# Performance work log

Hardware: AMD Instinct MI355X
Metric: run time of the kernel (lower is better)

## Reference

```python
import jax, jax.numpy as jnp
import numpy as np

B, T, E, A = 4, 4096, 512, 64

def setup_inputs() -> dict:
    key = jax.random.key(0)
    k1, k2, k3, k4 = jax.random.split(key, 4)
    embedded = jax.random.normal(k1, (B, T, E), dtype=jnp.float32)
    # torch Linear(E, A, bias=False): weight [A, E], y = x @ W.T. Store as [E, A].
    s = 1.0 / np.sqrt(E)
    Wq = jax.random.uniform(k2, (E, A), dtype=jnp.float32, minval=-s, maxval=s)
    Wk = jax.random.uniform(k3, (E, A), dtype=jnp.float32, minval=-s, maxval=s)
    Wv = jax.random.uniform(k4, (E, A), dtype=jnp.float32, minval=-s, maxval=s)
    return {"embedded": embedded, "Wq": Wq, "Wk": Wk, "Wv": Wv}

def reference(embedded, Wq, Wk, Wv):
    Q = embedded @ Wq  # [B, T, A]
    K = embedded @ Wk
    V = embedded @ Wv
    A_dim = V.shape[-1]
    scores = jnp.einsum('btd,bsd->bts', Q, K) / jnp.sqrt(jnp.float32(A_dim))  # [B, T, T]
    Tlen = scores.shape[-1]
    causal = jnp.tril(jnp.ones((Tlen, Tlen), dtype=bool))
    scores = jnp.where(causal, scores, -jnp.inf)
    attn = jax.nn.softmax(scores, axis=-1)
    out = jnp.einsum('bts,bsd->btd', attn, V)  # [B, T, A]
    return jnp.round(out, 4)
```

## Files before the change

kernel.cpp:

```cpp
#include <hip/hip_runtime.h>

#define B_ 4
#define T_ 4096
#define E_ 512
#define A_ 64
#define SQSCALE 0.1803368801111204f

typedef __attribute__((ext_vector_type(8)))  short bf16x8;
typedef __attribute__((ext_vector_type(8)))  unsigned short ushort8;
typedef __attribute__((ext_vector_type(4)))  unsigned int   u32x4;
typedef __attribute__((ext_vector_type(4)))  float f32x4;
typedef __attribute__((ext_vector_type(16))) float f32x16;

__device__ __forceinline__ unsigned short f2bf(float x) {
    union { float f; unsigned int u; } v; v.f = x;
    unsigned int r = v.u + 0x7fffu + ((v.u >> 16) & 1u);
    return (unsigned short)(r >> 16);
}
__device__ __forceinline__ unsigned cvtpk(float a, float b) {
    unsigned r;
    asm("v_cvt_pk_bf16_f32 %0, %1, %2" : "=v"(r) : "v"(a), "v"(b));
    return r;
}
__device__ __forceinline__ void pls(unsigned &a, unsigned &b) {
    asm("v_permlane32_swap_b32 %0, %1" : "+v"(a), "+v"(b));
}

__global__ __launch_bounds__(256) void prep_w(
    const float* __restrict__ Wq, const float* __restrict__ Wk,
    const float* __restrict__ Wv, unsigned short* __restrict__ Wp)
{
    const int e = blockIdx.x * 256 + threadIdx.x;
    const int nt = e >> 10;
    const int ks = (e >> 6) & 15;
    const int l  = e & 63;
    const int col = nt * 16 + (l & 15);
    const int kb  = ks * 32 + (l >> 4) * 8;
    const float* W = (col < 64) ? Wq : ((col < 128) ? Wk : Wv);
    const int cc = col & 63;
    const float sc = (col < 64) ? SQSCALE : 1.f;
    union { unsigned short s[8]; ushort8 v; } u;
    #pragma unroll
    for (int j = 0; j < 8; ++j) u.s[j] = f2bf(W[(kb + j) * 64 + cc] * sc);
    *(ushort8*)&Wp[(size_t)e * 8] = u.v;
}

__global__ __launch_bounds__(512, 4) void qkv_proj_kernel(
    const float* __restrict__ emb, const unsigned short* __restrict__ Wp,
    unsigned short* __restrict__ Qp, unsigned short* __restrict__ Kp,
    unsigned short* __restrict__ Vp)
{
    __shared__ unsigned short at[32][536];
    __shared__ unsigned short qt[32][72];
    __shared__ unsigned short kt[32][72];
    __shared__ unsigned short vt[64][40];
    const int tid = threadIdx.x;
    const long row0 = (long)blockIdx.x * 32;

    {
        const int r = tid >> 4, c16 = tid & 15;
        const float* __restrict__ src = emb + (row0 + r) * 512;
        #pragma unroll
        for (int j = 0; j < 4; ++j) {
            const int col = j * 128 + c16 * 8;
            const float4 x0 = *(const float4*)(src + col);
            const float4 x1 = *(const float4*)(src + col + 4);
            u32x4 p;
            p[0] = cvtpk(x0.x, x0.y); p[1] = cvtpk(x0.z, x0.w);
            p[2] = cvtpk(x1.x, x1.y); p[3] = cvtpk(x1.z, x1.w);
            *(u32x4*)&at[r][col] = p;
        }
    }
    __syncthreads();

    const int w = tid >> 6, lane = tid & 63;
    const int c = lane & 15, hi = lane >> 4;
    const int rg = w & 1, ng = w >> 1;

    f32x4 acc[3];
    #pragma unroll
    for (int j = 0; j < 3; ++j) acc[j] = (f32x4){0.f, 0.f, 0.f, 0.f};

    #pragma unroll
    for (int ks = 0; ks < 16; ++ks) {
        const bf16x8 af = *(const bf16x8*)&at[rg * 16 + c][ks * 32 + hi * 8];
        #pragma unroll
        for (int j = 0; j < 3; ++j) {
            const int nt = ng * 3 + j;
            const bf16x8 bf_ = *(const bf16x8*)&Wp[((size_t)(nt * 16 + ks) * 64 + lane) * 8];
            acc[j] = __builtin_amdgcn_mfma_f32_16x16x32_bf16(af, bf_, acc[j], 0, 0, 0);
        }
    }

    #pragma unroll
    for (int j = 0; j < 3; ++j) {
        const int nt = ng * 3 + j;
        #pragma unroll
        for (int r4 = 0; r4 < 4; ++r4) {
            const int rloc = rg * 16 + hi * 4 + r4;
            const unsigned short v = f2bf(acc[j][r4]);
            if (nt < 4)       qt[rloc][nt * 16 + c] = v;
            else if (nt < 8)  kt[rloc][(nt - 4) * 16 + c] = v;
            else              vt[(nt - 8) * 16 + c][rloc] = v;
        }
    }
    __syncthreads();

    const int tloc = (int)(row0 & 4095);
    const long bb = row0 >> 12;
    const int ci  = tloc >> 6;
    const int f_  = (tloc >> 5) & 1;
    const int ks0 = (tloc >> 4) & 3;
    const int tt  = tloc >> 5;
    if (tid < 256) {
        const int kk = tid >> 6, l = tid & 63;
        const ushort8 kval = *(const ushort8*)&kt[l & 31][kk * 16 + (l >> 5) * 8];
        *(ushort8*)&Kp[((((bb * 64 + ci) * 2 + f_) * 4 + kk) * 64 + l) * 8] = kval;
        const ushort8 qval = *(const ushort8*)&qt[l & 31][kk * 16 + (l >> 5) * 8];
        *(ushort8*)&Qp[(((bb * 128 + tt) * 4 + kk) * 64 + l) * 8] = qval;
    } else {
        const int e = tid - 256;
        const int ksl = e >> 7, ct = (e >> 6) & 1, l = e & 63;
        const ushort8 val = *(const ushort8*)&vt[ct * 32 + (l & 31)][ksl * 16 + (l >> 5) * 8];
        *(ushort8*)&Vp[((((bb * 64 + ci) * 4 + ks0 + ksl) * 2 + ct) * 64 + l) * 8] = val;
    }
}

__global__ __launch_bounds__(512, 2) void attn_kernel(
    const unsigned short* __restrict__ Qp, const unsigned short* __restrict__ Kp,
    const unsigned short* __restrict__ Vp, float* __restrict__ out)
{
    __shared__ float accbuf[8][32][68];
    __shared__ float mbuf[8][32], lbuf[8][32];

    const int tid = threadIdx.x, w = tid >> 6, lane = tid & 63;
    const int c = lane & 31, h = lane >> 5;
    const int b = (blockIdx.x & 7) >> 1;
    const int u = ((blockIdx.x >> 3) << 1) | (blockIdx.x & 1);
    const int t = (u < 64) ? (127 - u) : (u - 64);
    const int qb = t << 5;

    const unsigned short* __restrict__ Qpb = Qp + (size_t)b * 128 * 4 * 512;
    const unsigned short* __restrict__ Kpb = Kp + (size_t)b * 64 * 8 * 512;
    const unsigned short* __restrict__ Vpb = Vp + (size_t)b * 64 * 8 * 512;

    bf16x8 qf[4];
    #pragma unroll
    for (int kk = 0; kk < 4; ++kk)
        qf[kk] = *(const bf16x8*)&Qpb[(((size_t)t * 4 + kk) * 64 + lane) * 8];

    f32x16 acc[2];
    #pragma unroll
    for (int ct = 0; ct < 2; ++ct)
        #pragma unroll
        for (int j = 0; j < 16; ++j) acc[ct][j] = 0.f;
    float m = -1e30f, l = 0.f;

    const int nc = ((qb + 31) >> 6) + 1;

    bf16x8 kf[2][4];
    {
        const size_t cp = (w < nc) ? w : (nc - 1);
        #pragma unroll
        for (int f = 0; f < 2; ++f)
            #pragma unroll
            for (int kk = 0; kk < 4; ++kk)
                kf[f][kk] = *(const bf16x8*)&Kpb[(((cp * 2 + f) * 4 + kk) * 64 + lane) * 8];
    }

    for (int ci = w; ci < nc; ci += 8) {
        const long s0 = (long)ci << 6;

        bf16x8 vf[4][2];
        #pragma unroll
        for (int ks = 0; ks < 4; ++ks)
            #pragma unroll
            for (int ct = 0; ct < 2; ++ct)
                vf[ks][ct] = *(const bf16x8*)&Vpb[((((size_t)ci * 4 + ks) * 2 + ct) * 64 + lane) * 8];

        f32x16 sf[2];
        #pragma unroll
        for (int f = 0; f < 2; ++f)
            #pragma unroll
            for (int j = 0; j < 16; ++j) sf[f][j] = 0.f;
        __builtin_amdgcn_s_setprio(1);
        #pragma unroll
        for (int f = 0; f < 2; ++f)
            #pragma unroll
            for (int kk = 0; kk < 4; ++kk)
                sf[f] = __builtin_amdgcn_mfma_f32_32x32x16_bf16(kf[f][kk], qf[kk], sf[f], 0, 0, 0);
        __builtin_amdgcn_s_setprio(0);

        bf16x8 kn[2][4];
        {
            const int cin = ci + 8;
            const size_t cp = (cin < nc) ? cin : (nc - 1);
            #pragma unroll
            for (int f = 0; f < 2; ++f)
                #pragma unroll
                for (int kk = 0; kk < 4; ++kk)
                    kn[f][kk] = *(const bf16x8*)&Kpb[(((cp * 2 + f) * 4 + kk) * 64 + lane) * 8];
        }

        if ((int)s0 + 63 > qb) {
            #pragma unroll
            for (int f = 0; f < 2; ++f)
                #pragma unroll
                for (int r = 0; r < 16; ++r) {
                    const int key = (int)s0 + f * 32 + ((r & 3) + 8 * (r >> 2)) + 4 * h;
                    if (key > qb + c) sf[f][r] = -1e30f;
                }
        }

        float t0 = fmaxf(sf[0][0], sf[1][0]);
        float t1 = fmaxf(sf[0][1], sf[1][1]);
        float t2 = fmaxf(sf[0][2], sf[1][2]);
        float t3 = fmaxf(sf[0][3], sf[1][3]);
        #pragma unroll
        for (int r = 4; r < 16; r += 4) {
            t0 = fmaxf(t0, fmaxf(sf[0][r],     sf[1][r]));
            t1 = fmaxf(t1, fmaxf(sf[0][r + 1], sf[1][r + 1]));
            t2 = fmaxf(t2, fmaxf(sf[0][r + 2], sf[1][r + 2]));
            t3 = fmaxf(t3, fmaxf(sf[0][r + 3], sf[1][r + 3]));
        }
        float pm = fmaxf(fmaxf(t0, t1), fmaxf(t2, t3));
        pm = fmaxf(pm, __shfl_xor(pm, 32));

        float mn = m;
        if (__any(pm > m)) {
            mn = fmaxf(m, pm);
            const float sc = exp2f(m - mn);
            m = mn;
            l *= sc;
            #pragma unroll
            for (int ct = 0; ct < 2; ++ct)
                #pragma unroll
                for (int r = 0; r < 16; ++r) acc[ct][r] *= sc;
        }

        float s0a = 0.f, s1a = 0.f, s2a = 0.f, s3a = 0.f;
        #pragma unroll
        for (int f = 0; f < 2; ++f)
            #pragma unroll
            for (int r = 0; r < 16; r += 4) {
                float p0 = exp2f(sf[f][r] - mn);
                float p1 = exp2f(sf[f][r + 1] - mn);
                float p2 = exp2f(sf[f][r + 2] - mn);
                float p3 = exp2f(sf[f][r + 3] - mn);
                sf[f][r] = p0; sf[f][r + 1] = p1; sf[f][r + 2] = p2; sf[f][r + 3] = p3;
                s0a += p0; s1a += p1; s2a += p2; s3a += p3;
            }
        float rs = (s0a + s1a) + (s2a + s3a);
        rs += __shfl_xor(rs, 32);
        l += rs;

        #pragma unroll
        for (int f = 0; f < 2; ++f) {
            unsigned w01 = cvtpk(sf[f][0], sf[f][1]);
            unsigned w23 = cvtpk(sf[f][2], sf[f][3]);
            unsigned w45 = cvtpk(sf[f][4], sf[f][5]);
            unsigned w67 = cvtpk(sf[f][6], sf[f][7]);
            pls(w01, w45); pls(w23, w67);
            union { unsigned uu[4]; bf16x8 v; } pa0, pa1;
            pa0.uu[0] = w01; pa0.uu[1] = w23; pa0.uu[2] = w45; pa0.uu[3] = w67;
            unsigned x01 = cvtpk(sf[f][8],  sf[f][9]);
            unsigned x23 = cvtpk(sf[f][10], sf[f][11]);
            unsigned x45 = cvtpk(sf[f][12], sf[f][13]);
            unsigned x67 = cvtpk(sf[f][14], sf[f][15]);
            pls(x01, x45); pls(x23, x67);
            pa1.uu[0] = x01; pa1.uu[1] = x23; pa1.uu[2] = x45; pa1.uu[3] = x67;
            __builtin_amdgcn_s_setprio(1);
            #pragma unroll
            for (int ct = 0; ct < 2; ++ct) {
                acc[ct] = __builtin_amdgcn_mfma_f32_32x32x16_bf16(vf[2 * f][ct],     pa0.v, acc[ct], 0, 0, 0);
                acc[ct] = __builtin_amdgcn_mfma_f32_32x32x16_bf16(vf[2 * f + 1][ct], pa1.v, acc[ct], 0, 0, 0);
            }
            __builtin_amdgcn_s_setprio(0);
        }

        #pragma unroll
        for (int f = 0; f < 2; ++f)
            #pragma unroll
            for (int kk = 0; kk < 4; ++kk) kf[f][kk] = kn[f][kk];
    }

    if (h == 0) { mbuf[w][c] = m; lbuf[w][c] = l; }
    #pragma unroll
    for (int ct = 0; ct < 2; ++ct)
        #pragma unroll
        for (int g = 0; g < 4; ++g)
            *(float4*)&accbuf[w][c][ct * 32 + g * 8 + 4 * h] =
                make_float4(acc[ct][4 * g], acc[ct][4 * g + 1],
                            acc[ct][4 * g + 2], acc[ct][4 * g + 3]);
    __syncthreads();
    #pragma unroll
    for (int i = 0; i < 4; ++i) {
        const int e = tid + i * 512;
        const int q = e >> 6, d = e & 63;
        float ms = mbuf[0][q];
        #pragma unroll
        for (int wv = 1; wv < 8; ++wv) ms = fmaxf(ms, mbuf[wv][q]);
        float ls = 0.f, os = 0.f;
        #pragma unroll
        for (int wv = 0; wv < 8; ++wv) {
            const float e_ = exp2f(mbuf[wv][q] - ms);
            ls += lbuf[wv][q] * e_;
            os += accbuf[wv][q][d] * e_;
        }
        out[((long)b * T_ + qb + q) * 64 + d] = os / ls;
    }
}

extern "C" void kernel_launch(void* const* d_in, const int* in_sizes, int n_in,
                              void* d_out, int out_size, void* d_ws, size_t ws_size,
                              hipStream_t stream)
{
    const float* emb = (const float*)d_in[0];
    const float* Wq  = (const float*)d_in[1];
    const float* Wk  = (const float*)d_in[2];
    const float* Wv  = (const float*)d_in[3];
    float* out = (float*)d_out;

    unsigned short* Qp = (unsigned short*)d_ws;
    unsigned short* Kp = Qp + (size_t)B_ * T_ * A_;
    unsigned short* Vp = Kp + (size_t)B_ * T_ * A_;
    unsigned short* Wp = Vp + (size_t)B_ * T_ * A_;

    prep_w<<<dim3(48), dim3(256), 0, stream>>>(Wq, Wk, Wv, Wp);
    qkv_proj_kernel<<<dim3(512), dim3(512), 0, stream>>>(emb, Wp, Qp, Kp, Vp);
    attn_kernel<<<dim3(512), dim3(512), 0, stream>>>(Qp, Kp, Vp, out);
}
```

Measured before the change: 52.02 us.

## Split attention KV range across two blocks and merge partials in a separate kernel

Splits the attention kernel into a flash-decoding style split-K: 1024 blocks each cover alternating groups of 8 key chunks (stride 16), write unnormalized partial accumulators plus max and sum to workspace, and a new merge kernel combines the two halves. This is meant to improve load balance and occupancy over the causal triangle, where long query tiles dominated a 512-block grid. It drops the heavy-first tile ordering and adds an extra launch plus global round-trip of partials. Blocks for short query tiles in the second half may do no work yet still write partials with m=-1e30, l=0.

```diff
diff --git a/kernel.cpp b/kernel.cpp
--- a/kernel.cpp
+++ b/kernel.cpp
@@ -126,18 +126,20 @@
     }
 }
 
-__global__ __launch_bounds__(512, 2) void attn_kernel(
+__global__ __launch_bounds__(512, 2) void attn_part(
     const unsigned short* __restrict__ Qp, const unsigned short* __restrict__ Kp,
-    const unsigned short* __restrict__ Vp, float* __restrict__ out)
+    const unsigned short* __restrict__ Vp, float* __restrict__ Pacc,
+    float* __restrict__ Pml)
 {
     __shared__ float accbuf[8][32][68];
     __shared__ float mbuf[8][32], lbuf[8][32];
 
     const int tid = threadIdx.x, w = tid >> 6, lane = tid & 63;
     const int c = lane & 31, h = lane >> 5;
-    const int b = (blockIdx.x & 7) >> 1;
-    const int u = ((blockIdx.x >> 3) << 1) | (blockIdx.x & 1);
-    const int t = (u < 64) ? (127 - u) : (u - 64);
+    const int bid = blockIdx.x;
+    const int b = bid & 3;
+    const int t = (bid >> 2) & 127;
+    const int half = bid >> 9;
     const int qb = t << 5;
 
     const unsigned short* __restrict__ Qpb = Qp + (size_t)b * 128 * 4 * 512;
@@ -157,18 +159,19 @@
     float m = -1e30f, l = 0.f;
 
     const int nc = ((qb + 31) >> 6) + 1;
+    const int ci0 = half * 8 + w;
+
+    const unsigned short* kptr = Kpb + (size_t)ci0 * 4096 + lane * 8;
+    const unsigned short* vptr = Vpb + (size_t)ci0 * 4096 + lane * 8;
 
     bf16x8 kf[2][4];
-    {
-        const size_t cp = (w < nc) ? w : (nc - 1);
-        #pragma unroll
-        for (int f = 0; f < 2; ++f)
-            #pragma unroll
-            for (int kk = 0; kk < 4; ++kk)
-                kf[f][kk] = *(const bf16x8*)&Kpb[(((cp * 2 + f) * 4 + kk) * 64 + lane) * 8];
-    }
-
-    for (int ci = w; ci < nc; ci += 8) {
+    #pragma unroll
+    for (int f = 0; f < 2; ++f)
+        #pragma unroll
+        for (int kk = 0; kk < 4; ++kk)
+            kf[f][kk] = *(const bf16x8*)&kptr[f * 2048 + kk * 512];
+
+    for (int ci = ci0; ci < nc; ci += 16) {
         const long s0 = (long)ci << 6;
 
         bf16x8 vf[4][2];
@@ -176,7 +179,7 @@
         for (int ks = 0; ks < 4; ++ks)
             #pragma unroll
             for (int ct = 0; ct < 2; ++ct)
-                vf[ks][ct] = *(const bf16x8*)&Vpb[((((size_t)ci * 4 + ks) * 2 + ct) * 64 + lane) * 8];
+                vf[ks][ct] = *(const bf16x8*)&vptr[ks * 1024 + ct * 512];
 
         f32x16 sf[2];
         #pragma unroll
@@ -191,16 +194,13 @@
                 sf[f] = __builtin_amdgcn_mfma_f32_32x32x16_bf16(kf[f][kk], qf[kk], sf[f], 0, 0, 0);
         __builtin_amdgcn_s_setprio(0);
 
+        const unsigned short* knp = (ci + 16 < nc) ? (kptr + 65536) : kptr;
         bf16x8 kn[2][4];
-        {
-            const int cin = ci + 8;
-            const size_t cp = (cin < nc) ? cin : (nc - 1);
-            #pragma unroll
-            for (int f = 0; f < 2; ++f)
-                #pragma unroll
-                for (int kk = 0; kk < 4; ++kk)
-                    kn[f][kk] = *(const bf16x8*)&Kpb[(((cp * 2 + f) * 4 + kk) * 64 + lane) * 8];
-        }
+        #pragma unroll
+        for (int f = 0; f < 2; ++f)
+            #pragma unroll
+            for (int kk = 0; kk < 4; ++kk)
+                kn[f][kk] = *(const bf16x8*)&knp[f * 2048 + kk * 512];
 
         if ((int)s0 + 63 > qb) {
             #pragma unroll
@@ -282,6 +282,8 @@
         for (int f = 0; f < 2; ++f)
             #pragma unroll
             for (int kk = 0; kk < 4; ++kk) kf[f][kk] = kn[f][kk];
+        kptr += 65536;
+        vptr += 65536;
     }
 
     if (h == 0) { mbuf[w][c] = m; lbuf[w][c] = l; }
@@ -293,6 +295,8 @@
                 make_float4(acc[ct][4 * g], acc[ct][4 * g + 1],
                             acc[ct][4 * g + 2], acc[ct][4 * g + 3]);
     __syncthreads();
+    float* __restrict__ Pa = Pacc + (size_t)bid * 2048;
+    float* __restrict__ Pm = Pml + (size_t)bid * 64;
     #pragma unroll
     for (int i = 0; i < 4; ++i) {
         const int e = tid + i * 512;
@@ -307,7 +311,31 @@
             ls += lbuf[wv][q] * e_;
             os += accbuf[wv][q][d] * e_;
         }
-        out[((long)b * T_ + qb + q) * 64 + d] = os / ls;
+        Pa[e] = os;
+        if (d == 0) { Pm[q] = ms; Pm[32 + q] = ls; }
+    }
+}
+
+__global__ __launch_bounds__(256) void attn_merge(
+    const float* __restrict__ Pacc, const float* __restrict__ Pml,
+    float* __restrict__ out)
+{
+    const int j = blockIdx.x;
+    const int b = j & 3, t = j >> 2;
+    const int bid0 = t * 4 + b;
+    const int bid1 = 512 + t * 4 + b;
+    const int tid = threadIdx.x;
+    #pragma unroll
+    for (int k = 0; k < 8; ++k) {
+        const int e = tid + k * 256;
+        const int q = e >> 6, d = e & 63;
+        const float m0 = Pml[(size_t)bid0 * 64 + q], l0 = Pml[(size_t)bid0 * 64 + 32 + q];
+        const float m1 = Pml[(size_t)bid1 * 64 + q], l1 = Pml[(size_t)bid1 * 64 + 32 + q];
+        const float M = fmaxf(m0, m1);
+        const float e0 = exp2f(m0 - M), e1 = exp2f(m1 - M);
+        const float num = e0 * Pacc[(size_t)bid0 * 2048 + e] + e1 * Pacc[(size_t)bid1 * 2048 + e];
+        const float den = e0 * l0 + e1 * l1;
+        out[(((long)b * T_ + t * 32 + q) * 64) + d] = num / den;
     }
 }
 
@@ -325,8 +353,11 @@
     unsigned short* Kp = Qp + (size_t)B_ * T_ * A_;
     unsigned short* Vp = Kp + (size_t)B_ * T_ * A_;
     unsigned short* Wp = Vp + (size_t)B_ * T_ * A_;
+    float* Pacc = (float*)(Wp + 12288 * 8);
+    float* Pml  = Pacc + (size_t)1024 * 2048;
 
     prep_w<<<dim3(48), dim3(256), 0, stream>>>(Wq, Wk, Wv, Wp);
     qkv_proj_kernel<<<dim3(512), dim3(512), 0, stream>>>(emb, Wp, Qp, Kp, Vp);
-    attn_kernel<<<dim3(512), dim3(512), 0, stream>>>(Qp, Kp, Vp, out);
-}
+    attn_part<<<dim3(1024), dim3(512), 0, stream>>>(Qp, Kp, Vp, Pacc, Pml);
+    attn_merge<<<dim3(512), dim3(256), 0, stream>>>(Pacc, Pml, out);
+}
```

Result: slower. 63.46 us (+22.0%).
